# Kernel optimization log

Hardware: AMD Instinct MI355X
Metric: run time of the kernel (lower is better)

Reference implementation:

```python
import jax, jax.numpy as jnp
import numpy as np

SD = 64      # state_dim
EMO = 16     # emo_dim
D = SD + EMO # fractal node dim
C = SD       # quantum in/out channels
E = SD * 5   # MHA embed dim (320)
NH = 4       # MHA heads
HD = E // NH
F = D * 5    # flattened fractal node state
LIGHT = 500.0


def setup_inputs() -> dict:
    key = jax.random.key(0)
    ks = iter(jax.random.split(key, 48))
    def n(shape, s=0.02):
        return jax.random.normal(next(ks), shape, dtype=jnp.float32) * s
    return dict(
        node_states=jax.random.normal(next(ks), (27, SD, 5), dtype=jnp.float32),
        hist_state=jax.random.normal(next(ks), (27, SD, 5), dtype=jnp.float32),
        # CausalDiscoveryLayer params
        granger_W=n((2 * SD * 5, 1)), granger_b=jnp.zeros((1,), jnp.float32),
        mha_in_W=n((3 * E, E)), mha_in_b=jnp.zeros((3 * E,), jnp.float32),
        mha_out_W=n((E, E)), mha_out_b=jnp.zeros((E,), jnp.float32),
        # QuantumEntangledGNN params
        q_real=n((27, C), 0.01), q_imag=n((27, C), 0.01),
        ent_W1=n((2 * C, 64)), ent_b1=jnp.zeros((64,), jnp.float32),
        ent_W2=n((64, C)), ent_b2=jnp.zeros((C,), jnp.float32),
        meas_W=n((2 * C, C * 5)), meas_b=jnp.zeros((C * 5,), jnp.float32),
        # FractalGNN (depth 2, 27-ary): 729 leaves, 27 mid, 1 root
        leaf_states=n((729, D, 5), 0.01),
        mid_states=n((27, D, 5), 0.01),
        root_state=n((D, 5), 0.01),
        mid_agg_W=n((27, 27 * F, F)), mid_agg_b=jnp.zeros((27, F), jnp.float32),
        root_agg_W=n((27 * F, F)), root_agg_b=jnp.zeros((F,), jnp.float32),
        mid_up_W1=n((27, 2 * F, 64)), mid_up_b1=jnp.zeros((27, 64), jnp.float32),
        mid_up_W2=n((27, 64, F)), mid_up_b2=jnp.zeros((27, F), jnp.float32),
        root_up_W1=n((2 * F, 64)), root_up_b1=jnp.zeros((64,), jnp.float32),
        root_up_W2=n((64, F)), root_up_b2=jnp.zeros((F,), jnp.float32),
    )


def _forward(node_states, hist_state, granger_W, granger_b, mha_in_W, mha_in_b,
             mha_out_W, mha_out_b, q_real, q_imag, ent_W1, ent_b1, ent_W2, ent_b2,
             meas_W, meas_b, leaf_states, mid_states, root_state, mid_agg_W,
             mid_agg_b, root_agg_W, root_agg_b, mid_up_W1, mid_up_b1, mid_up_W2,
             mid_up_b2, root_up_W1, root_up_b1, root_up_W2, root_up_b2):
    # ---- CausalDiscoveryLayer ----
    h = hist_state.reshape(27, SD * 5)   # historical_states[-1][j].view(-1)
    x = node_states.reshape(27, SD * 5)  # node_states[i].view(-1)
    # pred_input[i, j] = cat(hist[j], node[i]) -> granger test, all 27x27 pairs
    pred = jnp.concatenate([
        jnp.broadcast_to(h[None, :, :], (27, 27, SD * 5)),
        jnp.broadcast_to(x[:, None, :], (27, 27, SD * 5))], axis=-1)
    scores = jax.nn.sigmoid(pred @ granger_W + granger_b)[..., 0]
    # .item() in original detaches -> stop_gradient; diagonal stays zero
    causal_adj = jax.lax.stop_gradient(scores * (1.0 - jnp.eye(27, dtype=scores.dtype)))
    hertz_w = jnp.clip(jnp.float32(LIGHT / 1000.0), 0.1, 1.0)
    qkv = x @ mha_in_W.T + mha_in_b
    q, k, v = jnp.split(qkv, 3, axis=-1)
    qh = q.reshape(27, NH, HD).transpose(1, 0, 2)  # [h, s, d]
    kh = k.reshape(27, NH, HD).transpose(1, 0, 2)
    vh = v.reshape(27, NH, HD).transpose(1, 0, 2)
    attn = jax.nn.softmax(jnp.einsum('hqd,hkd->hqk', qh, kh) / jnp.float32(HD) ** 0.5, axis=-1)
    o = jnp.einsum('hqk,hkd->hqd', attn, vh).transpose(1, 0, 2).reshape(27, E)
    attended = ((o @ mha_out_W.T + mha_out_b) * hertz_w).reshape(27, SD, 5)

    # ---- QuantumEntangledGNN (351 unordered pairs i<j) ----
    iu, ju = np.triu_indices(27, 1)
    comb = jnp.concatenate([q_real[iu], q_real[ju]], axis=-1)       # [351, 2C]
    ent = jax.nn.relu(comb @ ent_W1 + ent_b1) @ ent_W2 + ent_b2     # [351, C]
    s = q_real.sum(axis=1)
    coupling = jnp.exp(-jnp.abs(s[iu] - s[ju]) / (LIGHT + 1e-6))
    avg_ent = (ent * coupling[:, None]).mean(axis=0)                # [C]
    qr = q_real + avg_ent[None, :]
    qi = q_imag + avg_ent[None, :]
    measured = (jnp.concatenate([qr, qi], axis=-1) @ meas_W + meas_b).reshape(3, 3, 3, C, 5)

    # ---- FractalGNN: leaves are passthrough; 27 mid nodes update, then root ----
    child_flat = leaf_states.reshape(27, 27 * F)  # each mid node's 27 leaf children
    agg = jnp.einsum('nij,ni->nj', mid_agg_W, child_flat) + mid_agg_b  # [27, F]
    comb_m = jnp.concatenate([mid_states.reshape(27, F), agg], axis=-1)
    hid = jax.nn.relu(jnp.einsum('nij,ni->nj', mid_up_W1, comb_m) + mid_up_b1)
    upd = jnp.einsum('nij,ni->nj', mid_up_W2, hid) + mid_up_b2
    new_mid = mid_states + upd.reshape(27, D, 5)
    cf = new_mid.reshape(27 * F)
    agg_r = cf @ root_agg_W + root_agg_b
    comb_r = jnp.concatenate([root_state.reshape(F), agg_r], axis=-1)
    new_root = root_state + (jax.nn.relu(comb_r @ root_up_W1 + root_up_b1) @ root_up_W2 + root_up_b2).reshape(D, 5)

    return causal_adj, attended, measured, new_root


def reference(node_states, hist_state, granger_W, granger_b, mha_in_W, mha_in_b,
              mha_out_W, mha_out_b, q_real, q_imag, ent_W1, ent_b1, ent_W2, ent_b2,
              meas_W, meas_b, leaf_states, mid_states, root_state, mid_agg_W,
              mid_agg_b, root_agg_W, root_agg_b, mid_up_W1, mid_up_b1, mid_up_W2,
              mid_up_b2, root_up_W1, root_up_b1, root_up_W2, root_up_b2):
    return _forward(node_states, hist_state, granger_W, granger_b, mha_in_W,
                    mha_in_b, mha_out_W, mha_out_b, q_real, q_imag, ent_W1, ent_b1,
                    ent_W2, ent_b2, meas_W, meas_b, leaf_states, mid_states,
                    root_state, mid_agg_W, mid_agg_b, root_agg_W, root_agg_b,
                    mid_up_W1, mid_up_b1, mid_up_W2, mid_up_b2, root_up_W1,
                    root_up_b1, root_up_W2, root_up_b2)
```

## Files before the change

### kernel.cpp

```cpp
#include <hip/hip_runtime.h>
#include <math.h>

typedef float v4f __attribute__((ext_vector_type(4)));

#define SD 64
#define CC 64
#define EE 320
#define NH 4
#define HDM 80
#define NS 27
#define NPAIR 351

#define NCHUNK 54
#define AGG_BLKS (27 * NCHUNK)

#define WS_QKV   0
#define WS_O     25920
#define WS_ENT   34560
#define WS_AVG   57024
#define WS_MIDP  57088
#define WS_CF    1223488
#define WS_ROOTP 1234288


__device__ void dev_mid_agg(int blk, const float* __restrict__ W,
                            const float* __restrict__ leaf, float* __restrict__ partial) {
    int n = blk / NCHUNK, chunk = blk % NCHUNK;
    int t = threadIdx.x;
    if (t >= 200) return;
    int rp = t / 100, j4 = t % 100;
    const float* c = leaf + n * 10800 + chunk * 200;
    const v4f* Wr = (const v4f*)(W + (size_t)(n * 10800 + chunk * 200) * 400);
    v4f acc = (v4f)(0.0f);
    #pragma unroll 16
    for (int rr = 0; rr < 100; ++rr) {
        int r = 2 * rr + rp;
        float cv = c[r];
        v4f w = __builtin_nontemporal_load(&Wr[(size_t)r * 100 + j4]);
        acc += cv * w;
    }
    ((v4f*)(partial + (size_t)(blk * 2 + rp) * 400))[j4] = acc;
}

__device__ void dev_granger(int blk, const float* __restrict__ x, const float* __restrict__ h,
                            const float* __restrict__ gW, const float* __restrict__ gb,
                            float* __restrict__ out) {
    int idx = blk * 256 + threadIdx.x;
    if (idx >= NS * NS) return;
    int i = idx / NS, j = idx % NS;
    const float* hr = h + j * 320;
    const float* xr = x + i * 320;
    float acc = gb[0];
    for (int k = 0; k < 320; ++k) acc += hr[k] * gW[k] + xr[k] * gW[320 + k];
    float sig = 1.0f / (1.0f + expf(-acc));
    out[idx] = (i == j) ? 0.0f : sig;
}

__device__ void dev_qkv(int blk, const float* __restrict__ x, const float* __restrict__ W,
                        const float* __restrict__ b, float* __restrict__ qkv) {
    int idx = blk * 256 + threadIdx.x;
    if (idx >= NS * 960) return;
    int i = idx / 960, c = idx % 960;
    const float4* xr = (const float4*)(x + i * 320);
    const float4* wr = (const float4*)(W + (size_t)c * 320);
    float acc = b[c];
    #pragma unroll 8
    for (int k = 0; k < 80; ++k) {
        float4 a = xr[k], w = wr[k];
        acc += a.x * w.x + a.y * w.y + a.z * w.z + a.w * w.w;
    }
    qkv[idx] = acc;
}

__device__ void dev_ent(int blk, const float* __restrict__ q_real,
                        const float* __restrict__ W1, const float* __restrict__ b1,
                        const float* __restrict__ W2, const float* __restrict__ b2,
                        float* __restrict__ ent_scaled) {
    __shared__ float comb[2][128];
    __shared__ float hid[2][64];
    int t = threadIdx.x;
    int sub = t >> 7, lt = t & 127;
    int p = blk * 2 + sub;
    bool pv = (p < NPAIR);
    bool valid = pv && (lt < 64);
    int i = 0, jj = 0;
    if (pv) {
        int rem = p;
        while (rem >= 26 - i) { rem -= 26 - i; ++i; }
        jj = i + 1 + rem;
    }
    float qa = 0.f, qb = 0.f;
    if (valid) { qa = q_real[i * CC + lt]; qb = q_real[jj * CC + lt]; }
    float sa = qa, sb = qb;
    #pragma unroll
    for (int off = 32; off; off >>= 1) { sa += __shfl_xor(sa, off); sb += __shfl_xor(sb, off); }
    float coupling = expf(-fabsf(sa - sb) / (500.0f + 1e-6f));
    if (valid) { comb[sub][lt] = qa; comb[sub][64 + lt] = qb; }
    __syncthreads();
    if (valid) {
        float hs = b1[lt];
        for (int ii = 0; ii < 128; ++ii) hs += comb[sub][ii] * W1[ii * 64 + lt];
        hid[sub][lt] = fmaxf(hs, 0.0f);
    }
    __syncthreads();
    if (valid) {
        float e = b2[lt];
        for (int k = 0; k < 64; ++k) e += hid[sub][k] * W2[k * 64 + lt];
        ent_scaled[p * 64 + lt] = e * coupling;
    }
}

__global__ __launch_bounds__(256) void k_stage1(
    const float* __restrict__ mid_agg_W, const float* __restrict__ leaf,
    const float* __restrict__ node, const float* __restrict__ hist,
    const float* __restrict__ gW, const float* __restrict__ gb,
    const float* __restrict__ mha_in_W, const float* __restrict__ mha_in_b,
    const float* __restrict__ q_real,
    const float* __restrict__ ent_W1, const float* __restrict__ ent_b1,
    const float* __restrict__ ent_W2, const float* __restrict__ ent_b2,
    float* __restrict__ mid_partial, float* __restrict__ out_causal,
    float* __restrict__ qkv, float* __restrict__ ent_scaled) {
    int blk = blockIdx.x;
    if (blk < AGG_BLKS)          dev_mid_agg(blk, mid_agg_W, leaf, mid_partial);
    else if (blk < AGG_BLKS + 3) dev_granger(blk - AGG_BLKS, node, hist, gW, gb, out_causal);
    else if (blk < AGG_BLKS + 105) dev_qkv(blk - AGG_BLKS - 3, node, mha_in_W, mha_in_b, qkv);
    else                         dev_ent(blk - AGG_BLKS - 105, q_real, ent_W1, ent_b1, ent_W2, ent_b2, ent_scaled);
}


__device__ void dev_attn(int blk, const float* __restrict__ qkv, float* __restrict__ o) {
    int h = blk / NS, q = blk % NS;
    int t = threadIdx.x;
    __shared__ float sc[NS];
    __shared__ float at[NS];
    if (t < NS) {
        const float* qrow = qkv + q * 960 + h * HDM;
        const float* krow = qkv + t * 960 + EE + h * HDM;
        float s = 0.0f;
        for (int d = 0; d < HDM; ++d) s += qrow[d] * krow[d];
        sc[t] = s * 0.1118033988749895f;
    }
    __syncthreads();
    if (t < NS) {
        float m = -1e30f;
        for (int s2 = 0; s2 < NS; ++s2) m = fmaxf(m, sc[s2]);
        float sum = 0.0f;
        for (int s2 = 0; s2 < NS; ++s2) sum += expf(sc[s2] - m);
        at[t] = expf(sc[t] - m) / sum;
    }
    __syncthreads();
    if (t < HDM) {
        float acc = 0.0f;
        for (int s2 = 0; s2 < NS; ++s2) acc += at[s2] * qkv[s2 * 960 + 2 * EE + h * HDM + t];
        o[q * EE + h * HDM + t] = acc;
    }
}

__device__ void dev_avg(const float* __restrict__ ent_scaled, float* __restrict__ avg) {
    __shared__ float aacc[8][64];
    int t = threadIdx.x;
    int col = t & 63, grp = t >> 6;
    float s = 0.0f;
    for (int p = grp; p < NPAIR; p += 8) s += ent_scaled[p * 64 + col];
    aacc[grp][col] = s;
    __syncthreads();
    if (t < 64) {
        float a = 0.0f;
        #pragma unroll
        for (int g = 0; g < 8; ++g) a += aacc[g][t];
        avg[t] = a / (float)NPAIR;
    }
}

__device__ void dev_up_mlp(const float* __restrict__ comb ,
                           const float* __restrict__ W1, const float* __restrict__ b1,
                           const float* __restrict__ W2, const float* __restrict__ b2,
                           const float* __restrict__ base, float* __restrict__ outp,
                           float* __restrict__ s4f , float* __restrict__ hid ) {
    int t = threadIdx.x;
    {
        const float4* W1f = (const float4*)W1;
        int i0 = t >> 4;
        float4 a4 = make_float4(0.f, 0.f, 0.f, 0.f);
        #pragma unroll
        for (int it = 0; it < 25; ++it) {
            float4 w = W1f[t + 512 * it];
            float cv = comb[i0 + 32 * it];
            a4.x += cv * w.x; a4.y += cv * w.y; a4.z += cv * w.z; a4.w += cv * w.w;
        }
        ((float4*)s4f)[t] = a4;
    }
    __syncthreads();
    if (t < 64) {
        float hs = b1[t];
        int r = t >> 2, c = t & 3;
        #pragma unroll 8
        for (int g = 0; g < 32; ++g) hs += s4f[(r + 16 * g) * 4 + c];
        hid[t] = fmaxf(hs, 0.0f);
    }
    __syncthreads();
    __shared__ float racc[4][400];
    if (t < 400) {
        int g = t / 100, j4 = t % 100;
        const float4* W2f = (const float4*)W2;
        float4 a4 = make_float4(0.f, 0.f, 0.f, 0.f);
        #pragma unroll
        for (int m = 0; m < 16; ++m) {
            int k = g + 4 * m;
            float4 w = W2f[k * 100 + j4];
            float hv = hid[k];
            a4.x += hv * w.x; a4.y += hv * w.y; a4.z += hv * w.z; a4.w += hv * w.w;
        }
        ((float4*)&racc[g][0])[j4] = a4;
    }
    __syncthreads();
    if (t < 400) {
        float u = b2[t];
        #pragma unroll
        for (int g = 0; g < 4; ++g) u += racc[g][t];
        outp[t] = base[t] + u;
    }
}

__device__ void dev_mid_up(int n, const float* __restrict__ partial, const float* __restrict__ agg_b,
                           const float* __restrict__ mid_states,
                           const float* __restrict__ W1, const float* __restrict__ b1,
                           const float* __restrict__ W2, const float* __restrict__ b2,
                           float* __restrict__ cf) {
    __shared__ float comb[800];
    __shared__ float s4f[2048];
    __shared__ float hid[64];
    int t = threadIdx.x;
    if (t < 400) {
        float a = agg_b[n * 400 + t];
        const float* pp = partial + (size_t)(n * NCHUNK * 2) * 400 + t;
        #pragma unroll 12
        for (int s = 0; s < NCHUNK * 2; ++s) a += pp[s * 400];
        comb[400 + t] = a;
        comb[t] = mid_states[n * 400 + t];
    }
    __syncthreads();
    dev_up_mlp(comb, W1 + (size_t)n * 51200, b1 + n * 64, W2 + (size_t)n * 25600, b2 + n * 400,
               mid_states + n * 400, cf + n * 400, s4f, hid);
}

__global__ __launch_bounds__(512) void k_stage2(
    const float* __restrict__ qkv, float* __restrict__ o,
    const float* __restrict__ ent_scaled, float* __restrict__ avg,
    const float* __restrict__ mid_partial, const float* __restrict__ mid_agg_b,
    const float* __restrict__ mid_states,
    const float* __restrict__ mid_up_W1, const float* __restrict__ mid_up_b1,
    const float* __restrict__ mid_up_W2, const float* __restrict__ mid_up_b2,
    float* __restrict__ cf) {
    int blk = blockIdx.x;
    if (blk < 108)       dev_attn(blk, qkv, o);
    else if (blk == 108) dev_avg(ent_scaled, avg);
    else                 dev_mid_up(blk - 109, mid_partial, mid_agg_b, mid_states,
                                    mid_up_W1, mid_up_b1, mid_up_W2, mid_up_b2, cf);
}


__device__ void dev_proj(int blk, const float* __restrict__ o, const float* __restrict__ W,
                         const float* __restrict__ b, float* __restrict__ outp) {
    int idx = blk * 512 + threadIdx.x;
    if (idx >= NS * EE) return;
    int i = idx / EE, c = idx % EE;
    const float4* orow = (const float4*)(o + i * EE);
    const float4* wr = (const float4*)(W + (size_t)c * EE);
    float acc = b[c];
    #pragma unroll 8
    for (int k = 0; k < 80; ++k) {
        float4 a = orow[k], w = wr[k];
        acc += a.x * w.x + a.y * w.y + a.z * w.z + a.w * w.w;
    }
    outp[idx] = 0.5f * acc;
}

__device__ void dev_measured(int blk, const float* __restrict__ q_real, const float* __restrict__ q_imag,
                             const float* __restrict__ avg, const float* __restrict__ W,
                             const float* __restrict__ b, float* __restrict__ out) {
    int idx = blk * 512 + threadIdx.x;
    if (idx >= NS * EE) return;
    int i = idx / EE, c = idx % EE;
    float acc = b[c];
    #pragma unroll 8
    for (int k = 0; k < 64; ++k) {
        float a = avg[k];
        acc += (q_real[i * 64 + k] + a) * W[k * EE + c];
        acc += (q_imag[i * 64 + k] + a) * W[(64 + k) * EE + c];
    }
    out[idx] = acc;
}

__device__ void dev_root_partial(int chunk, const float* __restrict__ W, const float* __restrict__ cf,
                                 float* __restrict__ partial) {
    __shared__ float racc[5][400];
    int t = threadIdx.x;
    int rp = t / 100, j4 = t % 100;
    if (rp < 5) {
        const float* c = cf + chunk * 100;
        const v4f* Wr = (const v4f*)W + (size_t)(chunk * 100) * 100;
        v4f acc = (v4f)(0.0f);
        #pragma unroll
        for (int rr = 0; rr < 20; ++rr) {
            int r = 5 * rr + rp;
            float cv = c[r];
            v4f w = __builtin_nontemporal_load(&Wr[(size_t)r * 100 + j4]);
            acc += cv * w;
        }
        racc[rp][j4 * 4 + 0] = acc.x;
        racc[rp][j4 * 4 + 1] = acc.y;
        racc[rp][j4 * 4 + 2] = acc.z;
        racc[rp][j4 * 4 + 3] = acc.w;
    }
    __syncthreads();
    if (t < 400) {
        float a = 0.0f;
        #pragma unroll
        for (int g = 0; g < 5; ++g) a += racc[g][t];
        partial[chunk * 400 + t] = a;
    }
}

__global__ __launch_bounds__(512) void k_stage3(
    const float* __restrict__ o, const float* __restrict__ mha_out_W,
    const float* __restrict__ mha_out_b, float* __restrict__ out_att,
    const float* __restrict__ q_real, const float* __restrict__ q_imag,
    const float* __restrict__ avg, const float* __restrict__ meas_W,
    const float* __restrict__ meas_b, float* __restrict__ out_meas,
    const float* __restrict__ root_agg_W, const float* __restrict__ cf,
    float* __restrict__ root_partial) {
    int blk = blockIdx.x;
    if (blk < 17)       dev_proj(blk, o, mha_out_W, mha_out_b, out_att);
    else if (blk < 34)  dev_measured(blk - 17, q_real, q_imag, avg, meas_W, meas_b, out_meas);
    else                dev_root_partial(blk - 34, root_agg_W, cf, root_partial);
}

__global__ __launch_bounds__(512) void k_root(
    const float* __restrict__ partial, const float* __restrict__ agg_b,
    const float* __restrict__ root_state,
    const float* __restrict__ W1, const float* __restrict__ b1,
    const float* __restrict__ W2, const float* __restrict__ b2,
    float* __restrict__ out) {
    __shared__ float comb[800];
    __shared__ float s4f[2048];
    __shared__ float hid[64];
    int t = threadIdx.x;
    if (t < 400) {
        float a = agg_b[t];
        const float* pp = partial + t;
        #pragma unroll 12
        for (int s = 0; s < 108; ++s) a += pp[s * 400];
        comb[400 + t] = a;
        comb[t] = root_state[t];
    }
    __syncthreads();
    dev_up_mlp(comb, W1, b1, W2, b2, root_state, out, s4f, hid);
}

extern "C" void kernel_launch(void* const* d_in, const int* in_sizes, int n_in,
                              void* d_out, int out_size, void* d_ws, size_t ws_size,
                              hipStream_t stream) {
    const float* node       = (const float*)d_in[0];
    const float* hist       = (const float*)d_in[1];
    const float* gW         = (const float*)d_in[2];
    const float* gb         = (const float*)d_in[3];
    const float* mha_in_W   = (const float*)d_in[4];
    const float* mha_in_b   = (const float*)d_in[5];
    const float* mha_out_W  = (const float*)d_in[6];
    const float* mha_out_b  = (const float*)d_in[7];
    const float* q_real     = (const float*)d_in[8];
    const float* q_imag     = (const float*)d_in[9];
    const float* ent_W1     = (const float*)d_in[10];
    const float* ent_b1     = (const float*)d_in[11];
    const float* ent_W2     = (const float*)d_in[12];
    const float* ent_b2     = (const float*)d_in[13];
    const float* meas_W     = (const float*)d_in[14];
    const float* meas_b     = (const float*)d_in[15];
    const float* leaf       = (const float*)d_in[16];
    const float* mid_states = (const float*)d_in[17];
    const float* root_state = (const float*)d_in[18];
    const float* mid_agg_W  = (const float*)d_in[19];
    const float* mid_agg_b  = (const float*)d_in[20];
    const float* root_agg_W = (const float*)d_in[21];
    const float* root_agg_b = (const float*)d_in[22];
    const float* mid_up_W1  = (const float*)d_in[23];
    const float* mid_up_b1  = (const float*)d_in[24];
    const float* mid_up_W2  = (const float*)d_in[25];
    const float* mid_up_b2  = (const float*)d_in[26];
    const float* root_up_W1 = (const float*)d_in[27];
    const float* root_up_b1 = (const float*)d_in[28];
    const float* root_up_W2 = (const float*)d_in[29];
    const float* root_up_b2 = (const float*)d_in[30];

    float* ws          = (float*)d_ws;
    float* qkv         = ws + WS_QKV;
    float* o           = ws + WS_O;
    float* ent_scaled  = ws + WS_ENT;
    float* avg         = ws + WS_AVG;
    float* mid_partial = ws + WS_MIDP;
    float* cf          = ws + WS_CF;
    float* root_part   = ws + WS_ROOTP;

    float* out        = (float*)d_out;
    float* out_causal = out;
    float* out_att    = out + 729;
    float* out_meas   = out + 9369;
    float* out_root   = out + 18009;

    hipLaunchKernelGGL(k_stage1, dim3(AGG_BLKS + 105 + 176), dim3(256), 0, stream,
                       mid_agg_W, leaf, node, hist, gW, gb, mha_in_W, mha_in_b,
                       q_real, ent_W1, ent_b1, ent_W2, ent_b2,
                       mid_partial, out_causal, qkv, ent_scaled);

    hipLaunchKernelGGL(k_stage2, dim3(136), dim3(512), 0, stream,
                       qkv, o, ent_scaled, avg, mid_partial, mid_agg_b, mid_states,
                       mid_up_W1, mid_up_b1, mid_up_W2, mid_up_b2, cf);

    hipLaunchKernelGGL(k_stage3, dim3(142), dim3(512), 0, stream,
                       o, mha_out_W, mha_out_b, out_att,
                       q_real, q_imag, avg, meas_W, meas_b, out_meas,
                       root_agg_W, cf, root_part);

    hipLaunchKernelGGL(k_root, dim3(1), dim3(512), 0, stream,
                       root_part, root_agg_b, root_state,
                       root_up_W1, root_up_b1, root_up_W2, root_up_b2, out_root);
}
```

Measured before the change: 143.7 us.

## Merge stages 2-4 into one tail kernel with atomic-counter dependencies

Three dependent launches (attention/avg/mid-update, projection/measure/root-partial, root MLP) become a single 281-block kernel. Cross-block ordering now uses global atomic counters and spin-waits instead of kernel boundaries, with last-arriver reduction for the MLP hidden layers. Attention is fused with the output projection, the averaging is fused into the measurement blocks, and the mid/root MLPs are split across 4 blocks each with more blocks feeding the root aggregation. This removes launch gaps and spreads the serial MLP tails over more blocks. The spin-waits rely on producer blocks being scheduled, which holds at this grid size but risks deadlock otherwise.

```diff
diff --git a/kernel.cpp b/kernel.cpp
--- a/kernel.cpp
+++ b/kernel.cpp
@@ -6,8 +6,6 @@
 #define SD 64
 #define CC 64
 #define EE 320
-#define NH 4
-#define HDM 80
 #define NS 27
 #define NPAIR 351
 
@@ -15,31 +13,42 @@
 #define AGG_BLKS (27 * NCHUNK)
 
 #define WS_QKV   0
-#define WS_O     25920
-#define WS_ENT   34560
-#define WS_AVG   57024
-#define WS_MIDP  57088
-#define WS_CF    1223488
-#define WS_ROOTP 1234288
+#define WS_ENT   25920
+#define WS_MIDP  48384
+#define WS_CF    1214784
+#define WS_ROOTP 1225584
+#define WS_HPM   1311984
+#define WS_HPR   1318896
+#define WS_CTR   1319168
+
+__device__ __forceinline__ void spin_wait(int* ctr, int target) {
+    if (threadIdx.x == 0) {
+        while (__hip_atomic_load(ctr, __ATOMIC_ACQUIRE, __HIP_MEMORY_SCOPE_AGENT) < target)
+            __builtin_amdgcn_s_sleep(8);
+    }
+    __syncthreads();
+}
 
 
 __device__ void dev_mid_agg(int blk, const float* __restrict__ W,
                             const float* __restrict__ leaf, float* __restrict__ partial) {
+    __shared__ float c_l[200];
     int n = blk / NCHUNK, chunk = blk % NCHUNK;
     int t = threadIdx.x;
-    if (t >= 200) return;
-    int rp = t / 100, j4 = t % 100;
-    const float* c = leaf + n * 10800 + chunk * 200;
-    const v4f* Wr = (const v4f*)(W + (size_t)(n * 10800 + chunk * 200) * 400);
-    v4f acc = (v4f)(0.0f);
-    #pragma unroll 16
-    for (int rr = 0; rr < 100; ++rr) {
-        int r = 2 * rr + rp;
-        float cv = c[r];
-        v4f w = __builtin_nontemporal_load(&Wr[(size_t)r * 100 + j4]);
-        acc += cv * w;
-    }
-    ((v4f*)(partial + (size_t)(blk * 2 + rp) * 400))[j4] = acc;
+    if (t < 200) c_l[t] = leaf[n * 10800 + chunk * 200 + t];
+    __syncthreads();
+    if (t < 200) {
+        int rp = t / 100, j4 = t % 100;
+        const v4f* Wr = (const v4f*)(W + (size_t)(n * 10800 + chunk * 200) * 400);
+        v4f acc = (v4f)(0.0f);
+        #pragma unroll 16
+        for (int rr = 0; rr < 100; ++rr) {
+            int r = 2 * rr + rp;
+            v4f w = __builtin_nontemporal_load(&Wr[(size_t)r * 100 + j4]);
+            acc += c_l[r] * w;
+        }
+        ((v4f*)(partial + (size_t)(blk * 2 + rp) * 400))[j4] = acc;
+    }
 }
 
 __device__ void dev_granger(int blk, const float* __restrict__ x, const float* __restrict__ h,
@@ -119,243 +128,258 @@
     const float* __restrict__ ent_W1, const float* __restrict__ ent_b1,
     const float* __restrict__ ent_W2, const float* __restrict__ ent_b2,
     float* __restrict__ mid_partial, float* __restrict__ out_causal,
-    float* __restrict__ qkv, float* __restrict__ ent_scaled) {
+    float* __restrict__ qkv, float* __restrict__ ent_scaled,
+    int* __restrict__ ctrs) {
     int blk = blockIdx.x;
-    if (blk < AGG_BLKS)          dev_mid_agg(blk, mid_agg_W, leaf, mid_partial);
-    else if (blk < AGG_BLKS + 3) dev_granger(blk - AGG_BLKS, node, hist, gW, gb, out_causal);
+    if (blk == 0 && threadIdx.x >= 224) ctrs[threadIdx.x - 224] = 0;
+    if (blk < AGG_BLKS)            dev_mid_agg(blk, mid_agg_W, leaf, mid_partial);
+    else if (blk < AGG_BLKS + 3)   dev_granger(blk - AGG_BLKS, node, hist, gW, gb, out_causal);
     else if (blk < AGG_BLKS + 105) dev_qkv(blk - AGG_BLKS - 3, node, mha_in_W, mha_in_b, qkv);
-    else                         dev_ent(blk - AGG_BLKS - 105, q_real, ent_W1, ent_b1, ent_W2, ent_b2, ent_scaled);
-}
-
-
-__device__ void dev_attn(int blk, const float* __restrict__ qkv, float* __restrict__ o) {
-    int h = blk / NS, q = blk % NS;
-    int t = threadIdx.x;
-    __shared__ float sc[NS];
-    __shared__ float at[NS];
-    if (t < NS) {
-        const float* qrow = qkv + q * 960 + h * HDM;
-        const float* krow = qkv + t * 960 + EE + h * HDM;
+    else                           dev_ent(blk - AGG_BLKS - 105, q_real, ent_W1, ent_b1, ent_W2, ent_b2, ent_scaled);
+}
+
+
+__device__ void dev_attnproj(int q, const float* __restrict__ qkv,
+                             const float* __restrict__ Wout, const float* __restrict__ bout,
+                             float* __restrict__ out_att) {
+    __shared__ float sc[4][27];
+    __shared__ float at[4][27];
+    __shared__ __align__(16) float o_l[320];
+    int t = threadIdx.x;
+    if (t < 108) {
+        int h = t / 27, k = t % 27;
+        const float* qr = qkv + q * 960 + h * 80;
+        const float* kr = qkv + k * 960 + 320 + h * 80;
         float s = 0.0f;
-        for (int d = 0; d < HDM; ++d) s += qrow[d] * krow[d];
-        sc[t] = s * 0.1118033988749895f;
-    }
-    __syncthreads();
-    if (t < NS) {
+        #pragma unroll 8
+        for (int d = 0; d < 80; ++d) s += qr[d] * kr[d];
+        sc[h][k] = s * 0.1118033988749895f;
+    }
+    __syncthreads();
+    if (t < 4) {
         float m = -1e30f;
-        for (int s2 = 0; s2 < NS; ++s2) m = fmaxf(m, sc[s2]);
+        for (int k = 0; k < 27; ++k) m = fmaxf(m, sc[t][k]);
         float sum = 0.0f;
-        for (int s2 = 0; s2 < NS; ++s2) sum += expf(sc[s2] - m);
-        at[t] = expf(sc[t] - m) / sum;
-    }
-    __syncthreads();
-    if (t < HDM) {
+        for (int k = 0; k < 27; ++k) sum += expf(sc[t][k] - m);
+        float inv = 1.0f / sum;
+        for (int k = 0; k < 27; ++k) at[t][k] = expf(sc[t][k] - m) * inv;
+    }
+    __syncthreads();
+    for (int j = t; j < 320; j += 256) {
+        int h = j / 80;
         float acc = 0.0f;
-        for (int s2 = 0; s2 < NS; ++s2) acc += at[s2] * qkv[s2 * 960 + 2 * EE + h * HDM + t];
-        o[q * EE + h * HDM + t] = acc;
-    }
-}
-
-__device__ void dev_avg(const float* __restrict__ ent_scaled, float* __restrict__ avg) {
-    __shared__ float aacc[8][64];
-    int t = threadIdx.x;
-    int col = t & 63, grp = t >> 6;
+        for (int k = 0; k < 27; ++k) acc += at[h][k] * qkv[k * 960 + 640 + j];
+        o_l[j] = acc;
+    }
+    __syncthreads();
+    for (int j = t; j < 320; j += 256) {
+        const float4* wr = (const float4*)(Wout + (size_t)j * 320);
+        const float4* ol = (const float4*)o_l;
+        float acc = bout[j];
+        #pragma unroll 8
+        for (int k = 0; k < 80; ++k) {
+            float4 w = wr[k], a = ol[k];
+            acc += a.x * w.x + a.y * w.y + a.z * w.z + a.w * w.w;
+        }
+        out_att[q * 320 + j] = 0.5f * acc;
+    }
+}
+
+__device__ void dev_measured(int blk, const float* __restrict__ ent_scaled,
+                             const float* __restrict__ q_real, const float* __restrict__ q_imag,
+                             const float* __restrict__ W, const float* __restrict__ b,
+                             float* __restrict__ out) {
+    __shared__ float aac[4][64];
+    __shared__ float avg_l[64];
+    int t = threadIdx.x;
+    int col = t & 63, g = t >> 6;
     float s = 0.0f;
-    for (int p = grp; p < NPAIR; p += 8) s += ent_scaled[p * 64 + col];
-    aacc[grp][col] = s;
-    __syncthreads();
-    if (t < 64) {
-        float a = 0.0f;
-        #pragma unroll
-        for (int g = 0; g < 8; ++g) a += aacc[g][t];
-        avg[t] = a / (float)NPAIR;
-    }
-}
-
-__device__ void dev_up_mlp(const float* __restrict__ comb ,
-                           const float* __restrict__ W1, const float* __restrict__ b1,
-                           const float* __restrict__ W2, const float* __restrict__ b2,
-                           const float* __restrict__ base, float* __restrict__ outp,
-                           float* __restrict__ s4f , float* __restrict__ hid ) {
-    int t = threadIdx.x;
-    {
-        const float4* W1f = (const float4*)W1;
-        int i0 = t >> 4;
-        float4 a4 = make_float4(0.f, 0.f, 0.f, 0.f);
-        #pragma unroll
-        for (int it = 0; it < 25; ++it) {
-            float4 w = W1f[t + 512 * it];
-            float cv = comb[i0 + 32 * it];
-            a4.x += cv * w.x; a4.y += cv * w.y; a4.z += cv * w.z; a4.w += cv * w.w;
-        }
-        ((float4*)s4f)[t] = a4;
-    }
-    __syncthreads();
-    if (t < 64) {
-        float hs = b1[t];
-        int r = t >> 2, c = t & 3;
+    for (int p = g; p < NPAIR; p += 4) s += ent_scaled[p * 64 + col];
+    aac[g][col] = s;
+    __syncthreads();
+    if (t < 64) avg_l[t] = (aac[0][t] + aac[1][t] + aac[2][t] + aac[3][t]) / (float)NPAIR;
+    __syncthreads();
+    int idx = blk * 256 + t;
+    if (idx < NS * EE) {
+        int i = idx / EE, c = idx % EE;
+        float acc = b[c];
         #pragma unroll 8
-        for (int g = 0; g < 32; ++g) hs += s4f[(r + 16 * g) * 4 + c];
-        hid[t] = fmaxf(hs, 0.0f);
-    }
-    __syncthreads();
-    __shared__ float racc[4][400];
-    if (t < 400) {
-        int g = t / 100, j4 = t % 100;
-        const float4* W2f = (const float4*)W2;
-        float4 a4 = make_float4(0.f, 0.f, 0.f, 0.f);
-        #pragma unroll
-        for (int m = 0; m < 16; ++m) {
-            int k = g + 4 * m;
-            float4 w = W2f[k * 100 + j4];
-            float hv = hid[k];
-            a4.x += hv * w.x; a4.y += hv * w.y; a4.z += hv * w.z; a4.w += hv * w.w;
-        }
-        ((float4*)&racc[g][0])[j4] = a4;
-    }
-    __syncthreads();
-    if (t < 400) {
-        float u = b2[t];
-        #pragma unroll
-        for (int g = 0; g < 4; ++g) u += racc[g][t];
-        outp[t] = base[t] + u;
-    }
-}
-
-__device__ void dev_mid_up(int n, const float* __restrict__ partial, const float* __restrict__ agg_b,
+        for (int k = 0; k < 64; ++k) {
+            float a = avg_l[k];
+            acc += (q_real[i * 64 + k] + a) * W[k * EE + c];
+            acc += (q_imag[i * 64 + k] + a) * W[(64 + k) * EE + c];
+        }
+        out[idx] = acc;
+    }
+}
+
+__device__ void dev_mid_up(int rel, const float* __restrict__ partial, const float* __restrict__ agg_b,
                            const float* __restrict__ mid_states,
                            const float* __restrict__ W1, const float* __restrict__ b1,
                            const float* __restrict__ W2, const float* __restrict__ b2,
-                           float* __restrict__ cf) {
-    __shared__ float comb[800];
-    __shared__ float s4f[2048];
+                           float* __restrict__ cf, float* __restrict__ hpm, int* __restrict__ ctrs) {
+    int n = rel >> 2, p = rel & 3;
+    __shared__ float combq[200];
+    __shared__ float hp4[4][64];
     __shared__ float hid[64];
-    int t = threadIdx.x;
-    if (t < 400) {
-        float a = agg_b[n * 400 + t];
-        const float* pp = partial + (size_t)(n * NCHUNK * 2) * 400 + t;
-        #pragma unroll 12
-        for (int s = 0; s < NCHUNK * 2; ++s) a += pp[s * 400];
-        comb[400 + t] = a;
-        comb[t] = mid_states[n * 400 + t];
-    }
-    __syncthreads();
-    dev_up_mlp(comb, W1 + (size_t)n * 51200, b1 + n * 64, W2 + (size_t)n * 25600, b2 + n * 400,
-               mid_states + n * 400, cf + n * 400, s4f, hid);
-}
-
-__global__ __launch_bounds__(512) void k_stage2(
-    const float* __restrict__ qkv, float* __restrict__ o,
-    const float* __restrict__ ent_scaled, float* __restrict__ avg,
+    __shared__ int flag;
+    int t = threadIdx.x;
+    if (p < 2) {
+        if (t < 200) combq[t] = mid_states[n * 400 + p * 200 + t];
+    } else {
+        int j0 = (p - 2) * 200;
+        if (t < 200) {
+            float a = agg_b[n * 400 + j0 + t];
+            const float* pp = partial + (size_t)(n * 108) * 400 + j0 + t;
+            #pragma unroll 12
+            for (int s = 0; s < 108; ++s) a += pp[s * 400];
+            combq[t] = a;
+        }
+    }
+    __syncthreads();
+    {
+        int h = t & 63, g = t >> 6;
+        const float* w1 = W1 + (size_t)n * 51200 + (size_t)(p * 200) * 64;
+        float hs = 0.0f;
+        #pragma unroll 5
+        for (int i = g * 50; i < g * 50 + 50; ++i) hs += combq[i] * w1[i * 64 + h];
+        hp4[g][h] = hs;
+    }
+    __syncthreads();
+    if (t < 64) hpm[(n * 4 + p) * 64 + t] = hp4[0][t] + hp4[1][t] + hp4[2][t] + hp4[3][t];
+    __syncthreads();
+    if (t == 0) {
+        int old = __hip_atomic_fetch_add(&ctrs[n], 1, __ATOMIC_ACQ_REL, __HIP_MEMORY_SCOPE_AGENT);
+        flag = (old == 3);
+    }
+    __syncthreads();
+    if (flag) {
+        if (t < 64) {
+            float hs = b1[n * 64 + t];
+            #pragma unroll
+            for (int pq = 0; pq < 4; ++pq) hs += hpm[(n * 4 + pq) * 64 + t];
+            hid[t] = fmaxf(hs, 0.0f);
+        }
+        __syncthreads();
+        const float* w2 = W2 + (size_t)n * 25600;
+        for (int j = t; j < 400; j += 256) {
+            float u = b2[n * 400 + j];
+            #pragma unroll 8
+            for (int k = 0; k < 64; ++k) u += hid[k] * w2[k * 400 + j];
+            cf[n * 400 + j] = mid_states[n * 400 + j] + u;
+        }
+        __syncthreads();
+        if (t == 0) __hip_atomic_fetch_add(&ctrs[27], 1, __ATOMIC_ACQ_REL, __HIP_MEMORY_SCOPE_AGENT);
+    }
+}
+
+__device__ void dev_rootagg(int chunk, const float* __restrict__ W, const float* __restrict__ cf,
+                            float* __restrict__ partial_r, int* __restrict__ ctrs) {
+    spin_wait(&ctrs[27], 27);
+    __shared__ float c_l[100];
+    int t = threadIdx.x;
+    if (t < 100) c_l[t] = cf[chunk * 100 + t];
+    __syncthreads();
+    if (t < 200) {
+        int rp = t / 100, j4 = t % 100;
+        const v4f* Wr = (const v4f*)W + (size_t)(chunk * 100) * 100;
+        v4f acc = (v4f)(0.0f);
+        #pragma unroll 10
+        for (int rr = 0; rr < 50; ++rr) {
+            int r = 2 * rr + rp;
+            v4f w = __builtin_nontemporal_load(&Wr[(size_t)r * 100 + j4]);
+            acc += c_l[r] * w;
+        }
+        ((v4f*)(partial_r + (size_t)(chunk * 2 + rp) * 400))[j4] = acc;
+    }
+    __syncthreads();
+    if (t == 0) __hip_atomic_fetch_add(&ctrs[28], 1, __ATOMIC_ACQ_REL, __HIP_MEMORY_SCOPE_AGENT);
+}
+
+__device__ void dev_rootup(int qd, const float* __restrict__ partial_r, const float* __restrict__ agg_b,
+                           const float* __restrict__ root_state,
+                           const float* __restrict__ W1, const float* __restrict__ b1,
+                           const float* __restrict__ W2, const float* __restrict__ b2,
+                           float* __restrict__ out, float* __restrict__ hpr, int* __restrict__ ctrs) {
+    spin_wait(&ctrs[28], 108);
+    __shared__ float combq[200];
+    __shared__ float hp4[4][64];
+    __shared__ float hid[64];
+    __shared__ int flag;
+    int t = threadIdx.x;
+    if (qd < 2) {
+        if (t < 200) combq[t] = root_state[qd * 200 + t];
+    } else {
+        int j0 = (qd - 2) * 200;
+        if (t < 200) {
+            float a = agg_b[j0 + t];
+            const float* pp = partial_r + j0 + t;
+            #pragma unroll 12
+            for (int s = 0; s < 216; ++s) a += pp[s * 400];
+            combq[t] = a;
+        }
+    }
+    __syncthreads();
+    {
+        int h = t & 63, g = t >> 6;
+        const float* w1 = W1 + (size_t)(qd * 200) * 64;
+        float hs = 0.0f;
+        #pragma unroll 5
+        for (int i = g * 50; i < g * 50 + 50; ++i) hs += combq[i] * w1[i * 64 + h];
+        hp4[g][h] = hs;
+    }
+    __syncthreads();
+    if (t < 64) hpr[qd * 64 + t] = hp4[0][t] + hp4[1][t] + hp4[2][t] + hp4[3][t];
+    __syncthreads();
+    if (t == 0) {
+        int old = __hip_atomic_fetch_add(&ctrs[29], 1, __ATOMIC_ACQ_REL, __HIP_MEMORY_SCOPE_AGENT);
+        flag = (old == 3);
+    }
+    __syncthreads();
+    if (flag) {
+        if (t < 64) {
+            float hs = b1[t];
+            #pragma unroll
+            for (int pq = 0; pq < 4; ++pq) hs += hpr[pq * 64 + t];
+            hid[t] = fmaxf(hs, 0.0f);
+        }
+        __syncthreads();
+        for (int j = t; j < 400; j += 256) {
+            float u = b2[j];
+            #pragma unroll 8
+            for (int k = 0; k < 64; ++k) u += hid[k] * W2[k * 400 + j];
+            out[j] = root_state[j] + u;
+        }
+    }
+}
+
+__global__ __launch_bounds__(256) void k_tail(
+    const float* __restrict__ qkv, const float* __restrict__ mha_out_W,
+    const float* __restrict__ mha_out_b, float* __restrict__ out_att,
+    const float* __restrict__ ent_scaled, const float* __restrict__ q_real,
+    const float* __restrict__ q_imag, const float* __restrict__ meas_W,
+    const float* __restrict__ meas_b, float* __restrict__ out_meas,
     const float* __restrict__ mid_partial, const float* __restrict__ mid_agg_b,
     const float* __restrict__ mid_states,
     const float* __restrict__ mid_up_W1, const float* __restrict__ mid_up_b1,
     const float* __restrict__ mid_up_W2, const float* __restrict__ mid_up_b2,
-    float* __restrict__ cf) {
+    float* __restrict__ cf,
+    const float* __restrict__ root_agg_W, const float* __restrict__ root_agg_b,
+    const float* __restrict__ root_state,
+    const float* __restrict__ root_up_W1, const float* __restrict__ root_up_b1,
+    const float* __restrict__ root_up_W2, const float* __restrict__ root_up_b2,
+    float* __restrict__ out_root,
+    float* __restrict__ partial_r, float* __restrict__ hpm, float* __restrict__ hpr,
+    int* __restrict__ ctrs) {
     int blk = blockIdx.x;
-    if (blk < 108)       dev_attn(blk, qkv, o);
-    else if (blk == 108) dev_avg(ent_scaled, avg);
-    else                 dev_mid_up(blk - 109, mid_partial, mid_agg_b, mid_states,
-                                    mid_up_W1, mid_up_b1, mid_up_W2, mid_up_b2, cf);
-}
-
-
-__device__ void dev_proj(int blk, const float* __restrict__ o, const float* __restrict__ W,
-                         const float* __restrict__ b, float* __restrict__ outp) {
-    int idx = blk * 512 + threadIdx.x;
-    if (idx >= NS * EE) return;
-    int i = idx / EE, c = idx % EE;
-    const float4* orow = (const float4*)(o + i * EE);
-    const float4* wr = (const float4*)(W + (size_t)c * EE);
-    float acc = b[c];
-    #pragma unroll 8
-    for (int k = 0; k < 80; ++k) {
-        float4 a = orow[k], w = wr[k];
-        acc += a.x * w.x + a.y * w.y + a.z * w.z + a.w * w.w;
-    }
-    outp[idx] = 0.5f * acc;
-}
-
-__device__ void dev_measured(int blk, const float* __restrict__ q_real, const float* __restrict__ q_imag,
-                             const float* __restrict__ avg, const float* __restrict__ W,
-                             const float* __restrict__ b, float* __restrict__ out) {
-    int idx = blk * 512 + threadIdx.x;
-    if (idx >= NS * EE) return;
-    int i = idx / EE, c = idx % EE;
-    float acc = b[c];
-    #pragma unroll 8
-    for (int k = 0; k < 64; ++k) {
-        float a = avg[k];
-        acc += (q_real[i * 64 + k] + a) * W[k * EE + c];
-        acc += (q_imag[i * 64 + k] + a) * W[(64 + k) * EE + c];
-    }
-    out[idx] = acc;
-}
-
-__device__ void dev_root_partial(int chunk, const float* __restrict__ W, const float* __restrict__ cf,
-                                 float* __restrict__ partial) {
-    __shared__ float racc[5][400];
-    int t = threadIdx.x;
-    int rp = t / 100, j4 = t % 100;
-    if (rp < 5) {
-        const float* c = cf + chunk * 100;
-        const v4f* Wr = (const v4f*)W + (size_t)(chunk * 100) * 100;
-        v4f acc = (v4f)(0.0f);
-        #pragma unroll
-        for (int rr = 0; rr < 20; ++rr) {
-            int r = 5 * rr + rp;
-            float cv = c[r];
-            v4f w = __builtin_nontemporal_load(&Wr[(size_t)r * 100 + j4]);
-            acc += cv * w;
-        }
-        racc[rp][j4 * 4 + 0] = acc.x;
-        racc[rp][j4 * 4 + 1] = acc.y;
-        racc[rp][j4 * 4 + 2] = acc.z;
-        racc[rp][j4 * 4 + 3] = acc.w;
-    }
-    __syncthreads();
-    if (t < 400) {
-        float a = 0.0f;
-        #pragma unroll
-        for (int g = 0; g < 5; ++g) a += racc[g][t];
-        partial[chunk * 400 + t] = a;
-    }
-}
-
-__global__ __launch_bounds__(512) void k_stage3(
-    const float* __restrict__ o, const float* __restrict__ mha_out_W,
-    const float* __restrict__ mha_out_b, float* __restrict__ out_att,
-    const float* __restrict__ q_real, const float* __restrict__ q_imag,
-    const float* __restrict__ avg, const float* __restrict__ meas_W,
-    const float* __restrict__ meas_b, float* __restrict__ out_meas,
-    const float* __restrict__ root_agg_W, const float* __restrict__ cf,
-    float* __restrict__ root_partial) {
-    int blk = blockIdx.x;
-    if (blk < 17)       dev_proj(blk, o, mha_out_W, mha_out_b, out_att);
-    else if (blk < 34)  dev_measured(blk - 17, q_real, q_imag, avg, meas_W, meas_b, out_meas);
-    else                dev_root_partial(blk - 34, root_agg_W, cf, root_partial);
-}
-
-__global__ __launch_bounds__(512) void k_root(
-    const float* __restrict__ partial, const float* __restrict__ agg_b,
-    const float* __restrict__ root_state,
-    const float* __restrict__ W1, const float* __restrict__ b1,
-    const float* __restrict__ W2, const float* __restrict__ b2,
-    float* __restrict__ out) {
-    __shared__ float comb[800];
-    __shared__ float s4f[2048];
-    __shared__ float hid[64];
-    int t = threadIdx.x;
-    if (t < 400) {
-        float a = agg_b[t];
-        const float* pp = partial + t;
-        #pragma unroll 12
-        for (int s = 0; s < 108; ++s) a += pp[s * 400];
-        comb[400 + t] = a;
-        comb[t] = root_state[t];
-    }
-    __syncthreads();
-    dev_up_mlp(comb, W1, b1, W2, b2, root_state, out, s4f, hid);
+    if (blk < 27)        dev_attnproj(blk, qkv, mha_out_W, mha_out_b, out_att);
+    else if (blk < 61)   dev_measured(blk - 27, ent_scaled, q_real, q_imag, meas_W, meas_b, out_meas);
+    else if (blk < 169)  dev_mid_up(blk - 61, mid_partial, mid_agg_b, mid_states,
+                                    mid_up_W1, mid_up_b1, mid_up_W2, mid_up_b2, cf, hpm, ctrs);
+    else if (blk < 277)  dev_rootagg(blk - 169, root_agg_W, cf, partial_r, ctrs);
+    else                 dev_rootup(blk - 277, partial_r, root_agg_b, root_state,
+                                    root_up_W1, root_up_b1, root_up_W2, root_up_b2,
+                                    out_root, hpr, ctrs);
 }
 
 extern "C" void kernel_launch(void* const* d_in, const int* in_sizes, int n_in,
@@ -395,12 +419,13 @@
 
     float* ws          = (float*)d_ws;
     float* qkv         = ws + WS_QKV;
-    float* o           = ws + WS_O;
     float* ent_scaled  = ws + WS_ENT;
-    float* avg         = ws + WS_AVG;
     float* mid_partial = ws + WS_MIDP;
     float* cf          = ws + WS_CF;
-    float* root_part   = ws + WS_ROOTP;
+    float* partial_r   = ws + WS_ROOTP;
+    float* hpm         = ws + WS_HPM;
+    float* hpr         = ws + WS_HPR;
+    int*   ctrs        = (int*)(ws + WS_CTR);
 
     float* out        = (float*)d_out;
     float* out_causal = out;
@@ -411,18 +436,14 @@
     hipLaunchKernelGGL(k_stage1, dim3(AGG_BLKS + 105 + 176), dim3(256), 0, stream,
                        mid_agg_W, leaf, node, hist, gW, gb, mha_in_W, mha_in_b,
                        q_real, ent_W1, ent_b1, ent_W2, ent_b2,
-                       mid_partial, out_causal, qkv, ent_scaled);
-
-    hipLaunchKernelGGL(k_stage2, dim3(136), dim3(512), 0, stream,
-                       qkv, o, ent_scaled, avg, mid_partial, mid_agg_b, mid_states,
-                       mid_up_W1, mid_up_b1, mid_up_W2, mid_up_b2, cf);
-
-    hipLaunchKernelGGL(k_stage3, dim3(142), dim3(512), 0, stream,
-                       o, mha_out_W, mha_out_b, out_att,
-                       q_real, q_imag, avg, meas_W, meas_b, out_meas,
-                       root_agg_W, cf, root_part);
-
-    hipLaunchKernelGGL(k_root, dim3(1), dim3(512), 0, stream,
-                       root_part, root_agg_b, root_state,
-                       root_up_W1, root_up_b1, root_up_W2, root_up_b2, out_root);
-}
+                       mid_partial, out_causal, qkv, ent_scaled, ctrs);
+
+    hipLaunchKernelGGL(k_tail, dim3(281), dim3(256), 0, stream,
+                       qkv, mha_out_W, mha_out_b, out_att,
+                       ent_scaled, q_real, q_imag, meas_W, meas_b, out_meas,
+                       mid_partial, mid_agg_b, mid_states,
+                       mid_up_W1, mid_up_b1, mid_up_W2, mid_up_b2, cf,
+                       root_agg_W, root_agg_b, root_state,
+                       root_up_W1, root_up_b1, root_up_W2, root_up_b2, out_root,
+                       partial_r, hpm, hpr, ctrs);
+}
```

After: 167.7 us. 1.17x slower.

## Split mid/root up-MLPs across four blocks with atomic last-block finish

Applied to the files above, without the earlier changes.

Each mid-node and root update MLP, previously handled by one 512-thread block, is split into four blocks. Each block computes a quarter of the first-layer partial products and writes it to workspace, and an atomic counter lets the last arriving block do the ReLU and second layer. The mid aggregation also stages its leaf chunk in shared memory before the weight loop. The counters are zeroed in stage1, and the cost is extra global traffic plus a dependence on correct acquire-release ordering between blocks.

```diff
diff --git a/kernel.cpp b/kernel.cpp
--- a/kernel.cpp
+++ b/kernel.cpp
@@ -6,8 +6,6 @@
 #define SD 64
 #define CC 64
 #define EE 320
-#define NH 4
-#define HDM 80
 #define NS 27
 #define NPAIR 351
 
@@ -15,31 +13,34 @@
 #define AGG_BLKS (27 * NCHUNK)
 
 #define WS_QKV   0
-#define WS_O     25920
-#define WS_ENT   34560
-#define WS_AVG   57024
-#define WS_MIDP  57088
-#define WS_CF    1223488
-#define WS_ROOTP 1234288
+#define WS_ENT   25920
+#define WS_MIDP  48384
+#define WS_CF    1214784
+#define WS_ROOTP 1225584
+#define WS_HPM   1268784
+#define WS_HPR   1275696
+#define WS_CTR   1275968
 
 
 __device__ void dev_mid_agg(int blk, const float* __restrict__ W,
                             const float* __restrict__ leaf, float* __restrict__ partial) {
+    __shared__ float c_l[200];
     int n = blk / NCHUNK, chunk = blk % NCHUNK;
     int t = threadIdx.x;
-    if (t >= 200) return;
-    int rp = t / 100, j4 = t % 100;
-    const float* c = leaf + n * 10800 + chunk * 200;
-    const v4f* Wr = (const v4f*)(W + (size_t)(n * 10800 + chunk * 200) * 400);
-    v4f acc = (v4f)(0.0f);
-    #pragma unroll 16
-    for (int rr = 0; rr < 100; ++rr) {
-        int r = 2 * rr + rp;
-        float cv = c[r];
-        v4f w = __builtin_nontemporal_load(&Wr[(size_t)r * 100 + j4]);
-        acc += cv * w;
-    }
-    ((v4f*)(partial + (size_t)(blk * 2 + rp) * 400))[j4] = acc;
+    if (t < 200) c_l[t] = leaf[n * 10800 + chunk * 200 + t];
+    __syncthreads();
+    if (t < 200) {
+        int rp = t / 100, j4 = t % 100;
+        const v4f* Wr = (const v4f*)(W + (size_t)(n * 10800 + chunk * 200) * 400);
+        v4f acc = (v4f)(0.0f);
+        #pragma unroll 16
+        for (int rr = 0; rr < 100; ++rr) {
+            int r = 2 * rr + rp;
+            v4f w = __builtin_nontemporal_load(&Wr[(size_t)r * 100 + j4]);
+            acc += c_l[r] * w;
+        }
+        ((v4f*)(partial + (size_t)(blk * 2 + rp) * 400))[j4] = acc;
+    }
 }
 
 __device__ void dev_granger(int blk, const float* __restrict__ x, const float* __restrict__ h,
@@ -119,12 +120,14 @@
     const float* __restrict__ ent_W1, const float* __restrict__ ent_b1,
     const float* __restrict__ ent_W2, const float* __restrict__ ent_b2,
     float* __restrict__ mid_partial, float* __restrict__ out_causal,
-    float* __restrict__ qkv, float* __restrict__ ent_scaled) {
+    float* __restrict__ qkv, float* __restrict__ ent_scaled,
+    int* __restrict__ ctrs) {
     int blk = blockIdx.x;
-    if (blk < AGG_BLKS)          dev_mid_agg(blk, mid_agg_W, leaf, mid_partial);
-    else if (blk < AGG_BLKS + 3) dev_granger(blk - AGG_BLKS, node, hist, gW, gb, out_causal);
+    if (blk == 0 && threadIdx.x >= 224) ctrs[threadIdx.x - 224] = 0;
+    if (blk < AGG_BLKS)            dev_mid_agg(blk, mid_agg_W, leaf, mid_partial);
+    else if (blk < AGG_BLKS + 3)   dev_granger(blk - AGG_BLKS, node, hist, gW, gb, out_causal);
     else if (blk < AGG_BLKS + 105) dev_qkv(blk - AGG_BLKS - 3, node, mha_in_W, mha_in_b, qkv);
-    else                         dev_ent(blk - AGG_BLKS - 105, q_real, ent_W1, ent_b1, ent_W2, ent_b2, ent_scaled);
+    else                           dev_ent(blk - AGG_BLKS - 105, q_real, ent_W1, ent_b1, ent_W2, ent_b2, ent_scaled);
 }
 
 
@@ -134,10 +137,10 @@
     __shared__ float sc[NS];
     __shared__ float at[NS];
     if (t < NS) {
-        const float* qrow = qkv + q * 960 + h * HDM;
-        const float* krow = qkv + t * 960 + EE + h * HDM;
+        const float* qrow = qkv + q * 960 + h * 80;
+        const float* krow = qkv + t * 960 + EE + h * 80;
         float s = 0.0f;
-        for (int d = 0; d < HDM; ++d) s += qrow[d] * krow[d];
+        for (int d = 0; d < 80; ++d) s += qrow[d] * krow[d];
         sc[t] = s * 0.1118033988749895f;
     }
     __syncthreads();
@@ -149,10 +152,10 @@
         at[t] = expf(sc[t] - m) / sum;
     }
     __syncthreads();
-    if (t < HDM) {
+    if (t < 80) {
         float acc = 0.0f;
-        for (int s2 = 0; s2 < NS; ++s2) acc += at[s2] * qkv[s2 * 960 + 2 * EE + h * HDM + t];
-        o[q * EE + h * HDM + t] = acc;
+        for (int s2 = 0; s2 < NS; ++s2) acc += at[s2] * qkv[s2 * 960 + 2 * EE + h * 80 + t];
+        o[q * EE + h * 80 + t] = acc;
     }
 }
 
@@ -172,76 +175,67 @@
     }
 }
 
-__device__ void dev_up_mlp(const float* __restrict__ comb ,
-                           const float* __restrict__ W1, const float* __restrict__ b1,
-                           const float* __restrict__ W2, const float* __restrict__ b2,
-                           const float* __restrict__ base, float* __restrict__ outp,
-                           float* __restrict__ s4f , float* __restrict__ hid ) {
-    int t = threadIdx.x;
-    {
-        const float4* W1f = (const float4*)W1;
-        int i0 = t >> 4;
-        float4 a4 = make_float4(0.f, 0.f, 0.f, 0.f);
-        #pragma unroll
-        for (int it = 0; it < 25; ++it) {
-            float4 w = W1f[t + 512 * it];
-            float cv = comb[i0 + 32 * it];
-            a4.x += cv * w.x; a4.y += cv * w.y; a4.z += cv * w.z; a4.w += cv * w.w;
-        }
-        ((float4*)s4f)[t] = a4;
-    }
-    __syncthreads();
-    if (t < 64) {
-        float hs = b1[t];
-        int r = t >> 2, c = t & 3;
-        #pragma unroll 8
-        for (int g = 0; g < 32; ++g) hs += s4f[(r + 16 * g) * 4 + c];
-        hid[t] = fmaxf(hs, 0.0f);
-    }
-    __syncthreads();
-    __shared__ float racc[4][400];
-    if (t < 400) {
-        int g = t / 100, j4 = t % 100;
-        const float4* W2f = (const float4*)W2;
-        float4 a4 = make_float4(0.f, 0.f, 0.f, 0.f);
-        #pragma unroll
-        for (int m = 0; m < 16; ++m) {
-            int k = g + 4 * m;
-            float4 w = W2f[k * 100 + j4];
-            float hv = hid[k];
-            a4.x += hv * w.x; a4.y += hv * w.y; a4.z += hv * w.z; a4.w += hv * w.w;
-        }
-        ((float4*)&racc[g][0])[j4] = a4;
-    }
-    __syncthreads();
-    if (t < 400) {
-        float u = b2[t];
-        #pragma unroll
-        for (int g = 0; g < 4; ++g) u += racc[g][t];
-        outp[t] = base[t] + u;
-    }
-}
-
-__device__ void dev_mid_up(int n, const float* __restrict__ partial, const float* __restrict__ agg_b,
+__device__ void dev_mid_up(int rel, const float* __restrict__ partial, const float* __restrict__ agg_b,
                            const float* __restrict__ mid_states,
                            const float* __restrict__ W1, const float* __restrict__ b1,
                            const float* __restrict__ W2, const float* __restrict__ b2,
-                           float* __restrict__ cf) {
-    __shared__ float comb[800];
-    __shared__ float s4f[2048];
+                           float* __restrict__ cf, float* __restrict__ hpm, int* __restrict__ ctrs) {
+    int n = rel >> 2, p = rel & 3;
+    __shared__ float combq[200];
+    __shared__ float hp8[8][64];
     __shared__ float hid[64];
-    int t = threadIdx.x;
-    if (t < 400) {
-        float a = agg_b[n * 400 + t];
-        const float* pp = partial + (size_t)(n * NCHUNK * 2) * 400 + t;
-        #pragma unroll 12
-        for (int s = 0; s < NCHUNK * 2; ++s) a += pp[s * 400];
-        comb[400 + t] = a;
-        comb[t] = mid_states[n * 400 + t];
-    }
-    __syncthreads();
-    dev_up_mlp(comb, W1 + (size_t)n * 51200, b1 + n * 64, W2 + (size_t)n * 25600, b2 + n * 400,
-               mid_states + n * 400, cf + n * 400, s4f, hid);
+    __shared__ int flag;
+    int t = threadIdx.x;
+    if (p < 2) {
+        if (t < 200) combq[t] = mid_states[n * 400 + p * 200 + t];
+    } else {
+        int j0 = (p - 2) * 200;
+        if (t < 200) {
+            float a = agg_b[n * 400 + j0 + t];
+            const float* pp = partial + (size_t)(n * 108) * 400 + j0 + t;
+            #pragma unroll 12
+            for (int s = 0; s < 108; ++s) a += pp[s * 400];
+            combq[t] = a;
+        }
+    }
+    __syncthreads();
+    {
+        int h = t & 63, g = t >> 6;
+        const float* w1 = W1 + (size_t)n * 51200 + (size_t)(p * 200) * 64;
+        float hs = 0.0f;
+        #pragma unroll 5
+        for (int i = g * 25; i < g * 25 + 25; ++i) hs += combq[i] * w1[i * 64 + h];
+        hp8[g][h] = hs;
+    }
+    __syncthreads();
+    if (t < 64) {
+        float hs = 0.0f;
+        #pragma unroll
+        for (int g = 0; g < 8; ++g) hs += hp8[g][t];
+        hpm[(n * 4 + p) * 64 + t] = hs;
+    }
+    __syncthreads();
+    if (t == 0) {
+        int old = __hip_atomic_fetch_add(&ctrs[n], 1, __ATOMIC_ACQ_REL, __HIP_MEMORY_SCOPE_AGENT);
+        flag = (old == 3);
+    }
+    __syncthreads();
+    if (flag) {
+        if (t < 64) {
+            float hs = b1[n * 64 + t];
+            #pragma unroll
+            for (int pq = 0; pq < 4; ++pq) hs += hpm[(n * 4 + pq) * 64 + t];
+            hid[t] = fmaxf(hs, 0.0f);
+        }
+        __syncthreads();
+        const float* w2 = W2 + (size_t)n * 25600;
+        if (t < 400) {
+            float u = b2[n * 400 + t];
+            #pragma unroll 8
+            for (int k = 0; k < 64; ++k) u += hid[k] * w2[k * 400 + t];
+            cf[n * 400 + t] = mid_states[n * 400 + t] + u;
+        }
+    }
 }
 
 __global__ __launch_bounds__(512) void k_stage2(
@@ -251,12 +245,12 @@
     const float* __restrict__ mid_states,
     const float* __restrict__ mid_up_W1, const float* __restrict__ mid_up_b1,
     const float* __restrict__ mid_up_W2, const float* __restrict__ mid_up_b2,
-    float* __restrict__ cf) {
+    float* __restrict__ cf, float* __restrict__ hpm, int* __restrict__ ctrs) {
     int blk = blockIdx.x;
     if (blk < 108)       dev_attn(blk, qkv, o);
     else if (blk == 108) dev_avg(ent_scaled, avg);
     else                 dev_mid_up(blk - 109, mid_partial, mid_agg_b, mid_states,
-                                    mid_up_W1, mid_up_b1, mid_up_W2, mid_up_b2, cf);
+                                    mid_up_W1, mid_up_b1, mid_up_W2, mid_up_b2, cf, hpm, ctrs);
 }
 
 
@@ -292,8 +286,8 @@
     out[idx] = acc;
 }
 
-__device__ void dev_root_partial(int chunk, const float* __restrict__ W, const float* __restrict__ cf,
-                                 float* __restrict__ partial) {
+__device__ void dev_rootagg(int chunk, const float* __restrict__ W, const float* __restrict__ cf,
+                            float* __restrict__ partial_r) {
     __shared__ float racc[5][400];
     int t = threadIdx.x;
     int rp = t / 100, j4 = t % 100;
@@ -318,7 +312,7 @@
         float a = 0.0f;
         #pragma unroll
         for (int g = 0; g < 5; ++g) a += racc[g][t];
-        partial[chunk * 400 + t] = a;
+        partial_r[chunk * 400 + t] = a;
     }
 }
 
@@ -329,33 +323,74 @@
     const float* __restrict__ avg, const float* __restrict__ meas_W,
     const float* __restrict__ meas_b, float* __restrict__ out_meas,
     const float* __restrict__ root_agg_W, const float* __restrict__ cf,
-    float* __restrict__ root_partial) {
+    float* __restrict__ partial_r) {
     int blk = blockIdx.x;
     if (blk < 17)       dev_proj(blk, o, mha_out_W, mha_out_b, out_att);
     else if (blk < 34)  dev_measured(blk - 17, q_real, q_imag, avg, meas_W, meas_b, out_meas);
-    else                dev_root_partial(blk - 34, root_agg_W, cf, root_partial);
+    else                dev_rootagg(blk - 34, root_agg_W, cf, partial_r);
 }
 
 __global__ __launch_bounds__(512) void k_root(
-    const float* __restrict__ partial, const float* __restrict__ agg_b,
+    const float* __restrict__ partial_r, const float* __restrict__ agg_b,
     const float* __restrict__ root_state,
     const float* __restrict__ W1, const float* __restrict__ b1,
     const float* __restrict__ W2, const float* __restrict__ b2,
-    float* __restrict__ out) {
-    __shared__ float comb[800];
-    __shared__ float s4f[2048];
+    float* __restrict__ out, float* __restrict__ hpr, int* __restrict__ ctrs) {
+    int qd = blockIdx.x;
+    __shared__ float combq[200];
+    __shared__ float hp8[8][64];
     __shared__ float hid[64];
-    int t = threadIdx.x;
-    if (t < 400) {
-        float a = agg_b[t];
-        const float* pp = partial + t;
-        #pragma unroll 12
-        for (int s = 0; s < 108; ++s) a += pp[s * 400];
-        comb[400 + t] = a;
-        comb[t] = root_state[t];
-    }
-    __syncthreads();
-    dev_up_mlp(comb, W1, b1, W2, b2, root_state, out, s4f, hid);
+    __shared__ int flag;
+    int t = threadIdx.x;
+    if (qd < 2) {
+        if (t < 200) combq[t] = root_state[qd * 200 + t];
+    } else {
+        int j0 = (qd - 2) * 200;
+        if (t < 200) {
+            float a = agg_b[j0 + t];
+            const float* pp = partial_r + j0 + t;
+            #pragma unroll 12
+            for (int s = 0; s < 108; ++s) a += pp[s * 400];
+            combq[t] = a;
+        }
+    }
+    __syncthreads();
+    {
+        int h = t & 63, g = t >> 6;
+        const float* w1 = W1 + (size_t)(qd * 200) * 64;
+        float hs = 0.0f;
+        #pragma unroll 5
+        for (int i = g * 25; i < g * 25 + 25; ++i) hs += combq[i] * w1[i * 64 + h];
+        hp8[g][h] = hs;
+    }
+    __syncthreads();
+    if (t < 64) {
+        float hs = 0.0f;
+        #pragma unroll
+        for (int g = 0; g < 8; ++g) hs += hp8[g][t];
+        hpr[qd * 64 + t] = hs;
+    }
+    __syncthreads();
+    if (t == 0) {
+        int old = __hip_atomic_fetch_add(&ctrs[30], 1, __ATOMIC_ACQ_REL, __HIP_MEMORY_SCOPE_AGENT);
+        flag = (old == 3);
+    }
+    __syncthreads();
+    if (flag) {
+        if (t < 64) {
+            float hs = b1[t];
+            #pragma unroll
+            for (int pq = 0; pq < 4; ++pq) hs += hpr[pq * 64 + t];
+            hid[t] = fmaxf(hs, 0.0f);
+        }
+        __syncthreads();
+        if (t < 400) {
+            float u = b2[t];
+            #pragma unroll 8
+            for (int k = 0; k < 64; ++k) u += hid[k] * W2[k * 400 + t];
+            out[t] = root_state[t] + u;
+        }
+    }
 }
 
 extern "C" void kernel_launch(void* const* d_in, const int* in_sizes, int n_in,
@@ -395,12 +430,15 @@
 
     float* ws          = (float*)d_ws;
     float* qkv         = ws + WS_QKV;
-    float* o           = ws + WS_O;
     float* ent_scaled  = ws + WS_ENT;
-    float* avg         = ws + WS_AVG;
     float* mid_partial = ws + WS_MIDP;
     float* cf          = ws + WS_CF;
-    float* root_part   = ws + WS_ROOTP;
+    float* partial_r   = ws + WS_ROOTP;
+    float* hpm         = ws + WS_HPM;
+    float* hpr         = ws + WS_HPR;
+    int*   ctrs        = (int*)(ws + WS_CTR);
+
+    float* o = ws + WS_CTR + 32;
 
     float* out        = (float*)d_out;
     float* out_causal = out;
@@ -408,21 +446,23 @@
     float* out_meas   = out + 9369;
     float* out_root   = out + 18009;
 
+    float* avg = o + 8640;
+
     hipLaunchKernelGGL(k_stage1, dim3(AGG_BLKS + 105 + 176), dim3(256), 0, stream,
                        mid_agg_W, leaf, node, hist, gW, gb, mha_in_W, mha_in_b,
                        q_real, ent_W1, ent_b1, ent_W2, ent_b2,
-                       mid_partial, out_causal, qkv, ent_scaled);
-
-    hipLaunchKernelGGL(k_stage2, dim3(136), dim3(512), 0, stream,
+                       mid_partial, out_causal, qkv, ent_scaled, ctrs);
+
+    hipLaunchKernelGGL(k_stage2, dim3(217), dim3(512), 0, stream,
                        qkv, o, ent_scaled, avg, mid_partial, mid_agg_b, mid_states,
-                       mid_up_W1, mid_up_b1, mid_up_W2, mid_up_b2, cf);
+                       mid_up_W1, mid_up_b1, mid_up_W2, mid_up_b2, cf, hpm, ctrs);
 
     hipLaunchKernelGGL(k_stage3, dim3(142), dim3(512), 0, stream,
                        o, mha_out_W, mha_out_b, out_att,
                        q_real, q_imag, avg, meas_W, meas_b, out_meas,
-                       root_agg_W, cf, root_part);
-
-    hipLaunchKernelGGL(k_root, dim3(1), dim3(512), 0, stream,
-                       root_part, root_agg_b, root_state,
-                       root_up_W1, root_up_b1, root_up_W2, root_up_b2, out_root);
-}
+                       root_agg_W, cf, partial_r);
+
+    hipLaunchKernelGGL(k_root, dim3(4), dim3(512), 0, stream,
+                       partial_r, root_agg_b, root_state,
+                       root_up_W1, root_up_b1, root_up_W2, root_up_b2, out_root, hpr, ctrs);
+}
```

New measurement: 141.8 us. About the same (-1.4%).
